# Kernel tuning notes

Hardware: AMD Instinct MI355X
Metric: run time of the kernel (lower is better)

## Reference

```python
import jax, jax.numpy as jnp
import numpy as np

N_EVENTS = 16
N_SAMPLES = 2 ** 15          # 32768
STEP = 256                   # window_size // 2
LONG_WINDOW = 4096
LONG_COEFFS = LONG_WINDOW // 2 + 1   # 2049
LONG_STEP = LONG_WINDOW // 2         # 2048
LONG_FRAMES = N_SAMPLES // LONG_STEP # 16
N_FRAMES = N_SAMPLES // STEP         # 128
B = 8                                 # audio batch
BE = B * N_EVENTS                     # event batch = 128


def setup_inputs() -> dict:
    key = jax.random.key(0)
    k1, k2, k3, k4 = jax.random.split(key, 4)
    env = jax.random.uniform(k1, (BE, LONG_WINDOW, LONG_FRAMES), jnp.float32)
    tf = jax.random.normal(k2, (BE, LONG_COEFFS * 2, LONG_FRAMES), jnp.float32)
    noise = jax.random.uniform(k3, (BE, LONG_WINDOW, LONG_FRAMES), jnp.float32)
    indices = jax.random.randint(k4, (B, N_EVENTS), 0, N_FRAMES, dtype=jnp.int32)
    return {"env": env, "tf": tf, "noise": noise, "indices": indices}


def _event_render(env, tf, noise):
    # env, noise: (BE, LONG_WINDOW, LONG_FRAMES); tf: (BE, 2*LONG_COEFFS, LONG_FRAMES)
    batch = env.shape[0]
    energy = env * (noise * 2.0 - 1.0)  # uniform_(-1, 1) noise scaled by amp

    # magnitude = norm over interleaved (real, imag) pairs, per torch view semantics
    pairs = tf.reshape(batch, LONG_COEFFS, 2, LONG_FRAMES)
    mag = jnp.sqrt(jnp.sum(pairs * pairs, axis=2))  # (batch, C, F)
    mx = jnp.max(mag.reshape(batch, -1), axis=-1, keepdims=True)
    mag = (mag.reshape(batch, -1) / (mx + 1e-8)).reshape(batch, LONG_COEFFS, LONG_FRAMES)
    imag = tf[:, LONG_COEFFS:, :]
    phase = jnp.arctan2(imag, mag) * np.pi  # torch.angle(complex(mag, imag)) * pi
    tfc = mag * jnp.exp(1j * phase)         # complex transfer fn (batch, C, F)

    # sequential per-frame recurrence: state feeds through rfft/irfft filtering
    e_t = jnp.transpose(energy, (2, 0, 1))  # (F, batch, W)
    t_t = jnp.transpose(tfc, (2, 0, 1))     # (F, batch, C)

    def step(prev, inp):
        e, t = inp
        local = prev + e
        spec = jnp.fft.rfft(local, axis=-1, norm='ortho') * t
        frame = jnp.fft.irfft(spec, n=LONG_WINDOW, axis=-1, norm='ortho')
        return frame, frame

    init = jnp.zeros((batch, LONG_WINDOW), energy.dtype)
    _, frames = jax.lax.scan(step, init, (e_t, t_t))   # (F, batch, W)
    frames = jnp.transpose(frames, (1, 0, 2))          # (batch, F, W)

    # overlap-add with hop = LONG_STEP = W/2: split frames into halves and add
    halves = frames.reshape(batch, LONG_FRAMES, 2, LONG_STEP)
    out = jnp.zeros((batch, LONG_FRAMES + 1, LONG_STEP), frames.dtype)
    out = out.at[:, :LONG_FRAMES].add(halves[:, :, 0])
    out = out.at[:, 1:].add(halves[:, :, 1])
    return out.reshape(batch, -1)[:, :N_SAMPLES]       # (BE, N_SAMPLES)


def _segment_render(atoms, indices):
    # atoms: (BE, N_SAMPLES) -> (B, N_EVENTS, N_SAMPLES); scatter-add at time offsets
    x = atoms.reshape(B, N_EVENTS, N_SAMPLES)
    times = indices * STEP                                      # (B, E)
    pos = times[:, :, None] + jnp.arange(N_SAMPLES)[None, None, :]  # (B, E, S)
    out = jnp.zeros((B, 2 * N_SAMPLES), x.dtype)
    bidx = jnp.arange(B)[:, None, None]
    out = out.at[bidx, pos].add(x)
    return out[:, None, :N_SAMPLES]                             # (B, 1, N_SAMPLES)


def reference(env, tf, noise, indices):
    atoms = _event_render(env, tf, noise)
    return _segment_render(atoms, indices)
```

## Files before the change

kernel.cpp:

```cpp
#include <hip/hip_runtime.h>
#include <hip/hip_fp16.h>
#include <math.h>

#define TWO_PI 6.283185307179586f

#define OFF_F    0ull
#define OFF_E    4194304ull
#define OFF_MAXP 8390656ull
#define OFF_Z    8391680ull

__device__ __forceinline__ int swz(int n) { return n ^ ((n >> 5) & 31); }

__device__ __forceinline__ int permf(int k) {
    return ((k & 1) << 10) | (((k >> 1) & 3) << 8) | (((k >> 3) & 3) << 6)
         | (((k >> 5) & 3) << 4) | (((k >> 7) & 3) << 2) | ((k >> 9) & 3);
}
__device__ __forceinline__ int perm8(int k) {
    return ((k & 7) << 8) | (((k >> 3) & 3) << 6) | (((k >> 5) & 3) << 4)
         | (((k >> 7) & 3) << 2) | ((k >> 9) & 3);
}

__device__ __forceinline__ float2 uph(unsigned u) {
    __half2 h = *(__half2*)&u;
    return __half22float2(h);
}
__device__ __forceinline__ unsigned pkh(float x, float y) {
    __half2 h = __floats2half2_rn(x, y);
    return *(unsigned*)&h;
}

__device__ __forceinline__ void r4f_core(float* cr, float* ci, int p0, int p1, int p2, int p3,
                                         float c1, float s1, float c2, float s2, float c3, float s3) {
    float ar = cr[p0], ai = ci[p0];
    float br = cr[p1], bi = ci[p1];
    float crr = cr[p2], cri = ci[p2];
    float drr = cr[p3], dri = ci[p3];
    float u0r = ar + crr, u0i = ai + cri;
    float u1r = ar - crr, u1i = ai - cri;
    float u2r = br + drr, u2i = bi + dri;
    float u3r = br - drr, u3i = bi - dri;
    cr[p0] = u0r + u2r; ci[p0] = u0i + u2i;
    float z1r = u1r + u3i, z1i = u1i - u3r;
    cr[p1] = z1r * c1 + z1i * s1; ci[p1] = z1i * c1 - z1r * s1;
    float z2r = u0r - u2r, z2i = u0i - u2i;
    cr[p2] = z2r * c2 + z2i * s2; ci[p2] = z2i * c2 - z2r * s2;
    float z3r = u1r - u3i, z3i = u1i + u3r;
    cr[p3] = z3r * c3 + z3i * s3; ci[p3] = z3i * c3 - z3r * s3;
}

__device__ __forceinline__ void r4i_pk(unsigned* b, int p0, int p1, int p2, int p3,
                                       float c1, float s1, float c2, float s2, float c3, float s3) {
    float2 z0 = uph(b[p0]), z1 = uph(b[p1]), z2 = uph(b[p2]), z3 = uph(b[p3]);
    float t1r = z1.x * c1 - z1.y * s1, t1i = z1.y * c1 + z1.x * s1;
    float t2r = z2.x * c2 - z2.y * s2, t2i = z2.y * c2 + z2.x * s2;
    float t3r = z3.x * c3 - z3.y * s3, t3i = z3.y * c3 + z3.x * s3;
    float u0r = z0.x + t2r, u0i = z0.y + t2i;
    float u1r = z0.x - t2r, u1i = z0.y - t2i;
    float u2r = t1r + t3r, u2i = t1i + t3i;
    float u3r = t1r - t3r, u3i = t1i - t3i;
    b[p0] = pkh(u0r + u2r, u0i + u2i);
    b[p1] = pkh(u1r - u3i, u1i + u3r);
    b[p2] = pkh(u0r - u2r, u0i - u2i);
    b[p3] = pkh(u1r + u3i, u1i - u3r);
}

#define STAGE4X(CORE, JEXPR, H, ANGEXPR)                                       \
    {                                                                          \
        _Pragma("unroll")                                                      \
        for (int half_ = 0; half_ < 2; ++half_) {                              \
            int b_ = tid + half_ * 1024;                                       \
            int i_ = b_ & 511;                                                 \
            float* cr_ = B + (b_ >> 9) * 4096;                                 \
            float* ci_ = cr_ + 2048;                                           \
            int j_ = (JEXPR);                                                  \
            int p0 = swz(j_), p1 = swz(j_ + (H)), p2 = swz(j_ + 2 * (H)),      \
                p3 = swz(j_ + 3 * (H));                                        \
            float s1, c1; __sincosf((ANGEXPR), &s1, &c1);                      \
            float c2 = c1 * c1 - s1 * s1, s2 = 2.f * c1 * s1;                  \
            float c3 = c1 * c2 - s1 * s2, s3 = s1 * c2 + c1 * s2;              \
            CORE(cr_, ci_, p0, p1, p2, p3, c1, s1, c2, s2, c3, s3);            \
        }                                                                      \
    }                                                                          \
    __syncthreads();

#define STAGE4P(JEXPR, H, ANGEXPR)                                             \
    {                                                                          \
        _Pragma("unroll")                                                      \
        for (int half_ = 0; half_ < 2; ++half_) {                              \
            int b_ = tid + half_ * 1024;                                       \
            int i_ = b_ & 511;                                                 \
            unsigned* bb_ = B2 + (b_ >> 9) * 2048;                             \
            int j_ = (JEXPR);                                                  \
            int p0 = swz(j_), p1 = swz(j_ + (H)), p2 = swz(j_ + 2 * (H)),      \
                p3 = swz(j_ + 3 * (H));                                        \
            float s1, c1; __sincosf((ANGEXPR), &s1, &c1);                      \
            float c2 = c1 * c1 - s1 * s1, s2 = 2.f * c1 * s1;                  \
            float c3 = c1 * c2 - s1 * s2, s3 = s1 * c2 + c1 * s2;              \
            r4i_pk(bb_, p0, p1, p2, p3, c1, s1, c2, s2, c3, s3);               \
        }                                                                      \
    }                                                                          \
    __syncthreads();

__global__ __launch_bounds__(1024, 8) void k_fwd(const float* __restrict__ env,
                                                 const float* __restrict__ noise,
                                                 const float* __restrict__ tf,
                                                 float* __restrict__ ws) {
    __shared__ float B[16384];
    int tid = threadIdx.x;
    int id = blockIdx.x;
    int xcd = id & 7, slot = id >> 3;
    int be = xcd * 16 + (slot >> 2);
    int fg = slot & 3;
    const float4* env4 = (const float4*)env;
    const float4* noi4 = (const float4*)noise;
    size_t base = (size_t)be * 16384 + fg;
#pragma unroll
    for (int it = 0; it < 4; ++it) {
        int n = it * 1024 + tid;
        float4 e = env4[base + (size_t)n * 4];
        float4 z = noi4[base + (size_t)n * 4];
        float v0 = e.x * (z.x * 2.0f - 1.0f);
        float v1 = e.y * (z.y * 2.0f - 1.0f);
        float v2 = e.z * (z.z * 2.0f - 1.0f);
        float v3 = e.w * (z.w * 2.0f - 1.0f);
        int m = swz(n >> 1) + (n & 1) * 2048;
        B[m] = v0; B[4096 + m] = v1; B[8192 + m] = v2; B[12288 + m] = v3;
    }
    __syncthreads();
    {
        int buf = tid >> 8, j = tid & 255;
        float* cr = B + buf * 4096;
        float* ci = cr + 2048;
        int p[8];
#pragma unroll
        for (int m = 0; m < 8; ++m) p[m] = swz(j + 256 * m);
        float xr[8], xi[8];
#pragma unroll
        for (int m = 0; m < 8; ++m) { xr[m] = cr[p[m]]; xi[m] = ci[p[m]]; }
        float t0r = xr[0] + xr[4], t0i = xi[0] + xi[4];
        float t1r = xr[0] - xr[4], t1i = xi[0] - xi[4];
        float t2r = xr[2] + xr[6], t2i = xi[2] + xi[6];
        float t3r = xr[2] - xr[6], t3i = xi[2] - xi[6];
        float A0r = t0r + t2r, A0i = t0i + t2i;
        float A2r = t0r - t2r, A2i = t0i - t2i;
        float A1r = t1r + t3i, A1i = t1i - t3r;
        float A3r = t1r - t3i, A3i = t1i + t3r;
        float u0r = xr[1] + xr[5], u0i = xi[1] + xi[5];
        float u1r = xr[1] - xr[5], u1i = xi[1] - xi[5];
        float u2r = xr[3] + xr[7], u2i = xi[3] + xi[7];
        float u3r = xr[3] - xr[7], u3i = xi[3] - xi[7];
        float B0r = u0r + u2r, B0i = u0i + u2i;
        float B2r = u0r - u2r, B2i = u0i - u2i;
        float B1r = u1r + u3i, B1i = u1i - u3r;
        float B3r = u1r - u3i, B3i = u1i + u3r;
        const float RH = 0.70710678118654752f;
        float b1r = (B1r + B1i) * RH, b1i = (B1i - B1r) * RH;
        float b2r = B2i, b2i = -B2r;
        float b3r = (B3i - B3r) * RH, b3i = -(B3r + B3i) * RH;
        float yr[8], yi[8];
        yr[0] = A0r + B0r; yi[0] = A0i + B0i; yr[4] = A0r - B0r; yi[4] = A0i - B0i;
        yr[1] = A1r + b1r; yi[1] = A1i + b1i; yr[5] = A1r - b1r; yi[5] = A1i - b1i;
        yr[2] = A2r + b2r; yi[2] = A2i + b2i; yr[6] = A2r - b2r; yi[6] = A2i - b2i;
        yr[3] = A3r + b3r; yi[3] = A3i + b3i; yr[7] = A3r - b3r; yi[7] = A3i - b3i;
        float s1, c1; __sincosf((float)j * (TWO_PI / 2048.0f), &s1, &c1);
        float wr = c1, wi = -s1;
        float cwr = wr, cwi = wi;
        cr[p[0]] = yr[0]; ci[p[0]] = yi[0];
#pragma unroll
        for (int m = 1; m < 8; ++m) {
            cr[p[m]] = yr[m] * cwr - yi[m] * cwi;
            ci[p[m]] = yr[m] * cwi + yi[m] * cwr;
            if (m < 7) {
                float nr = cwr * wr - cwi * wi;
                cwi = cwr * wi + cwi * wr;
                cwr = nr;
            }
        }
    }
    __syncthreads();
    STAGE4X(r4f_core, (i_ >> 6) * 256 + (i_ & 63), 64, (float)(i_ & 63) * (TWO_PI / 256.0f));
    STAGE4X(r4f_core, (i_ & 31) * 64 + (i_ >> 5), 16, (float)(i_ >> 5) * (TWO_PI / 64.0f));
    STAGE4X(r4f_core, (i_ & 127) * 16 + (i_ >> 7), 4, (float)(i_ >> 7) * (TWO_PI / 16.0f));
    STAGE4X(r4f_core, i_ * 4, 1, 0.0f);
    __half2* Ebase = (__half2*)(ws + OFF_E) + (size_t)(be * 16 + fg * 4) * 2049;
    for (int k = tid; k <= 1024; k += 1024) {
        int pk = swz(perm8(k));
        int pm = swz(perm8((2048 - k) & 2047));
        float s4, c4; __sincosf((float)k * (TWO_PI / 4096.0f), &s4, &c4);
#pragma unroll
        for (int j4 = 0; j4 < 4; ++j4) {
            float* cr = B + j4 * 4096;
            float* ci = cr + 2048;
            float zkr = cr[pk], zki = ci[pk], zmr = cr[pm], zmi = ci[pm];
            float xer = 0.5f * (zkr + zmr), xei = 0.5f * (zki - zmi);
            float xor_ = 0.5f * (zki + zmi), xoi = 0.5f * (zmr - zkr);
            float wr = xor_ * c4 + xoi * s4;
            float wi = xoi * c4 - xor_ * s4;
            __half2* Eg = Ebase + (size_t)j4 * 2049;
            Eg[k] = __floats2half2_rn(xer + wr, xei + wi);
            Eg[2048 - k] = __floats2half2_rn(xer - wr, wi - xei);
        }
    }
    __syncthreads();
    const float4* ab4 = (const float4*)(tf + (size_t)be * 65568);
    int b0 = fg * 513;
    int nb = (fg == 3) ? 510 : 513;
    float mx = 0.f;
    for (int u = tid; u < nb * 4; u += 1024) {
        int g = u >> 2, e = u & 3;
        int bin = b0 + g;
        float4 A = ab4[bin * 8 + e];
        float4 Bv = ab4[bin * 8 + e + 4];
        mx = fmaxf(mx, fmaxf(fmaxf(A.x * A.x + Bv.x * Bv.x, A.y * A.y + Bv.y * Bv.y),
                             fmaxf(A.z * A.z + Bv.z * Bv.z, A.w * A.w + Bv.w * Bv.w)));
    }
#pragma unroll
    for (int off = 32; off > 0; off >>= 1)
        mx = fmaxf(mx, __shfl_xor(mx, off));
    if ((tid & 63) == 0) B[tid >> 6] = mx;
    __syncthreads();
    if (tid == 0) {
        float m = B[0];
#pragma unroll
        for (int i = 1; i < 16; ++i) m = fmaxf(m, B[i]);
        ws[OFF_MAXP + be * 4 + fg] = m;
    }
}

__global__ __launch_bounds__(256) void k_recur(const float* __restrict__ tf,
                                               float* __restrict__ ws) {
    __shared__ float sm2lo[256 * 17], simlo[256 * 17];
    __shared__ float sm2hi[256 * 17], simhi[256 * 17];
    int tid = threadIdx.x;
    int be = blockIdx.y;
    int k0 = blockIdx.x << 8;
    int hi0 = 1793 - k0;
    const float* tfb = tf + (size_t)be * 65568;
    const float4* ab4 = (const float4*)tfb;
    const float4* im4 = (const float4*)(tfb + 32784);

    for (int u = tid; u < 2048; u += 256) {
        int half = u >> 10, v = u & 1023;
        int g = v >> 2, e = v & 3;
        int bin = half ? (hi0 + g) : (k0 + g);
        float4 A = ab4[bin * 8 + e];
        float4 Bv = ab4[bin * 8 + e + 4];
        float4 I = im4[bin * 4 + e];
        int o = g * 17 + e * 4;
        float* sm = half ? sm2hi : sm2lo;
        float* si = half ? simhi : simlo;
        sm[o + 0] = A.x * A.x + Bv.x * Bv.x;
        sm[o + 1] = A.y * A.y + Bv.y * Bv.y;
        sm[o + 2] = A.z * A.z + Bv.z * Bv.z;
        sm[o + 3] = A.w * A.w + Bv.w * Bv.w;
        si[o + 0] = I.x; si[o + 1] = I.y; si[o + 2] = I.z; si[o + 3] = I.w;
    }
    __syncthreads();

    int k = k0 + tid;
    int m = 2048 - k;
    int rhi = 255 - tid;
    const float* mp = ws + OFF_MAXP + be * 4;
    float m2x = fmaxf(fmaxf(mp[0], mp[1]), fmaxf(mp[2], mp[3]));
    float rden = 1.0f / (sqrtf(m2x) + 1e-8f);
    const __half2* Eb = (const __half2*)(ws + OFF_E) + (size_t)be * 16 * 2049;
    __half2* Zb = (__half2*)(ws + OFF_Z) + (size_t)be * 16 * 2048;
    float2 evlo[16], evhi[16];
#pragma unroll
    for (int f = 0; f < 16; ++f) {
        evlo[f] = __half22float2(Eb[(size_t)f * 2049 + k]);
        evhi[f] = __half22float2(Eb[(size_t)f * 2049 + m]);
    }
    float ym = (k == 0) ? 0.0f : 1.0f;
    float s4, c4; __sincosf((float)k * (TWO_PI / 4096.0f), &s4, &c4);
    const float SCL = 1.0f / 2048.0f;
    float srl = 0.f, sil = 0.f, srh = 0.f, sih = 0.f;
#pragma unroll
    for (int f = 0; f < 16; ++f) {
        float mh = sqrtf(sm2lo[tid * 17 + f]) * rden;
        float ph = atan2f(simlo[tid * 17 + f], mh) * 3.14159265358979f;
        float sp, cp; __sincosf(ph, &sp, &cp);
        float Tr = mh * cp, Ti = mh * sp;
        sil *= ym;
        srl += evlo[f].x; sil += evlo[f].y;
        float nr = srl * Tr - sil * Ti;
        sil = srl * Ti + sil * Tr; srl = nr;
        float mh2 = sqrtf(sm2hi[rhi * 17 + f]) * rden;
        float ph2 = atan2f(simhi[rhi * 17 + f], mh2) * 3.14159265358979f;
        float sp2, cp2; __sincosf(ph2, &sp2, &cp2);
        float Tr2 = mh2 * cp2, Ti2 = mh2 * sp2;
        sih *= ym;
        srh += evhi[f].x; sih += evhi[f].y;
        float nr2 = srh * Tr2 - sih * Ti2;
        sih = srh * Ti2 + sih * Tr2; srh = nr2;
        __half2* Zf = Zb + (size_t)f * 2048;
        if (k == 0) {
            float y0 = srl * SCL, yn = srh * SCL;
            Zf[0] = __floats2half2_rn(0.5f * (y0 + yn), 0.5f * (y0 - yn));
        } else {
            float ykr = srl * SCL, yki = sil * SCL;
            float ymr = srh * SCL, ymi = sih * SCL;
            float er = 0.5f * (ykr + ymr), ei = 0.5f * (yki - ymi);
            float dr = ykr - ymr, di = yki + ymi;
            float orr = 0.5f * (dr * c4 - di * s4);
            float oi = 0.5f * (dr * s4 + di * c4);
            Zf[k] = __floats2half2_rn(er - oi, ei + orr);
            Zf[m] = __floats2half2_rn(er + oi, orr - ei);
        }
    }
    if (k0 == 0 && tid == 0) {
        float sr = 0.f, si = 0.f;
#pragma unroll
        for (int f = 0; f < 16; ++f) {
            float a = tfb[1024 * 32 + f];
            float b = tfb[1024 * 32 + 16 + f];
            float im = tfb[32784 + 1024 * 16 + f];
            float mh = sqrtf(a * a + b * b) * rden;
            float ph = atan2f(im, mh) * 3.14159265358979f;
            float sp, cp; __sincosf(ph, &sp, &cp);
            float Tr = mh * cp, Ti = mh * sp;
            float2 e = __half22float2(Eb[(size_t)f * 2049 + 1024]);
            sr += e.x; si += e.y;
            float nr = sr * Tr - si * Ti;
            si = sr * Ti + si * Tr; sr = nr;
            Zb[(size_t)f * 2048 + 1024] = __floats2half2_rn(sr * SCL, -si * SCL);
        }
    }
}

__global__ __launch_bounds__(1024, 8) void k_fft_inv(float* __restrict__ ws) {
    __shared__ unsigned B2[8192];
    int tid = threadIdx.x;
    int be = blockIdx.x >> 2, fg = blockIdx.x & 3;
    const __half2* Zbase = (const __half2*)(ws + OFF_Z) + (size_t)(be * 16 + fg * 4) * 2048;
    {
        int n0 = tid * 2;
        int p0 = swz(permf(n0)), p1 = swz(permf(n0 + 1));
#pragma unroll
        for (int j4 = 0; j4 < 4; ++j4) {
            uint2 raw = ((const uint2*)(Zbase + (size_t)j4 * 2048))[tid];
            unsigned* bb = B2 + j4 * 2048;
            bb[p0] = raw.x;
            bb[p1] = raw.y;
        }
    }
    __syncthreads();
    STAGE4P(i_ * 4, 1, 0.0f);
    STAGE4P((i_ & 127) * 16 + (i_ >> 7), 4, (float)(i_ >> 7) * (TWO_PI / 16.0f));
    STAGE4P((i_ & 31) * 64 + (i_ >> 5), 16, (float)(i_ >> 5) * (TWO_PI / 64.0f));
    STAGE4P((i_ >> 6) * 256 + (i_ & 63), 64, (float)(i_ & 63) * (TWO_PI / 256.0f));
    STAGE4P((i_ >> 8) * 1024 + (i_ & 255), 256, (float)(i_ & 255) * (TWO_PI / 1024.0f));
    {
        int sj = swz(tid), sjb = swz(tid + 1024);
        float s, c; __sincosf((float)tid * (TWO_PI / 2048.0f), &s, &c);
        __half2* Fbase = (__half2*)(ws + OFF_F) + (size_t)(be * 16 + fg * 4) * 2048;
#pragma unroll
        for (int j4 = 0; j4 < 4; ++j4) {
            unsigned* bb = B2 + j4 * 2048;
            float2 a = uph(bb[sj]);
            float2 b = uph(bb[sjb]);
            float tr = b.x * c - b.y * s, ti2 = b.x * s + b.y * c;
            __half2* Fg = Fbase + (size_t)j4 * 2048;
            Fg[tid] = __floats2half2_rn(a.x + tr, a.y + ti2);
            Fg[tid + 1024] = __floats2half2_rn(a.x - tr, a.y - ti2);
        }
    }
}

__global__ __launch_bounds__(256) void k_segment(const float* __restrict__ ws,
                                                 const int* __restrict__ indices,
                                                 float* __restrict__ out) {
    __shared__ int ste[16];
    int tid = threadIdx.x;
    int b = blockIdx.y;
    if (tid < 16) ste[tid] = indices[b * 16 + tid] * 256;
    __syncthreads();
    int g = blockIdx.x * 256 + tid;
    int t = g << 2;
    const __half* F = (const __half*)(ws + OFF_F);
    float4 acc = make_float4(0.f, 0.f, 0.f, 0.f);
#pragma unroll
    for (int e = 0; e < 16; ++e) {
        int te = ste[e];
        if (t >= te) {
            int d = t - te;
            int j = d >> 11, r = d & 2047;
            size_t base = (size_t)(b * 16 + e) * 65536;
            uint2 raw = *(const uint2*)(F + base + j * 4096 + r);
            float2 a0 = __half22float2(*(const __half2*)&raw.x);
            float2 a1 = __half22float2(*(const __half2*)&raw.y);
            acc.x += a0.x; acc.y += a0.y; acc.z += a1.x; acc.w += a1.y;
            if (j >= 1) {
                uint2 rw2 = *(const uint2*)(F + base + (j - 1) * 4096 + 2048 + r);
                float2 b0 = __half22float2(*(const __half2*)&rw2.x);
                float2 b1 = __half22float2(*(const __half2*)&rw2.y);
                acc.x += b0.x; acc.y += b0.y; acc.z += b1.x; acc.w += b1.y;
            }
        }
    }
    ((float4*)out)[(size_t)b * 8192 + g] = acc;
}

extern "C" void kernel_launch(void* const* d_in, const int* in_sizes, int n_in,
                              void* d_out, int out_size, void* d_ws, size_t ws_size,
                              hipStream_t stream) {
    const float* env = (const float*)d_in[0];
    const float* tf = (const float*)d_in[1];
    const float* noise = (const float*)d_in[2];
    const int* indices = (const int*)d_in[3];
    float* ws = (float*)d_ws;
    float* out = (float*)d_out;

    k_fwd<<<dim3(512), dim3(1024), 0, stream>>>(env, noise, tf, ws);
    k_recur<<<dim3(4, 128), dim3(256), 0, stream>>>(tf, ws);
    k_fft_inv<<<dim3(512), dim3(1024), 0, stream>>>(ws);
    k_segment<<<dim3(32, 8), dim3(256), 0, stream>>>(ws, indices, out);
}
```

Measured before the change: 74.08 us.

## Split forward FFT kernel into 1024 blocks of 512 threads handling two frames each

```diff
diff --git a/kernel.cpp b/kernel.cpp
--- a/kernel.cpp
+++ b/kernel.cpp
@@ -64,11 +64,11 @@
     b[p3] = pkh(u1r + u3i, u1i - u3r);
 }
 
-#define STAGE4X(CORE, JEXPR, H, ANGEXPR)                                       \
+#define STAGE2F(JEXPR, H, ANGEXPR)                                             \
     {                                                                          \
         _Pragma("unroll")                                                      \
         for (int half_ = 0; half_ < 2; ++half_) {                              \
-            int b_ = tid + half_ * 1024;                                       \
+            int b_ = tid + half_ * 512;                                        \
             int i_ = b_ & 511;                                                 \
             float* cr_ = B + (b_ >> 9) * 4096;                                 \
             float* ci_ = cr_ + 2048;                                           \
@@ -78,7 +78,7 @@
             float s1, c1; __sincosf((ANGEXPR), &s1, &c1);                      \
             float c2 = c1 * c1 - s1 * s1, s2 = 2.f * c1 * s1;                  \
             float c3 = c1 * c2 - s1 * s2, s3 = s1 * c2 + c1 * s2;              \
-            CORE(cr_, ci_, p0, p1, p2, p3, c1, s1, c2, s2, c3, s3);            \
+            r4f_core(cr_, ci_, p0, p1, p2, p3, c1, s1, c2, s2, c3, s3);        \
         }                                                                      \
     }                                                                          \
     __syncthreads();
@@ -101,30 +101,30 @@
     }                                                                          \
     __syncthreads();
 
-__global__ __launch_bounds__(1024, 8) void k_fwd(const float* __restrict__ env,
-                                                 const float* __restrict__ noise,
-                                                 const float* __restrict__ tf,
-                                                 float* __restrict__ ws) {
-    __shared__ float B[16384];
+__global__ __launch_bounds__(512, 8) void k_fwd(const float* __restrict__ env,
+                                                const float* __restrict__ noise,
+                                                const float* __restrict__ tf,
+                                                float* __restrict__ ws) {
+    __shared__ float B[8192];
     int tid = threadIdx.x;
     int id = blockIdx.x;
     int xcd = id & 7, slot = id >> 3;
-    int be = xcd * 16 + (slot >> 2);
-    int fg = slot & 3;
+    int be = xcd * 16 + (slot >> 3);
+    int fh = slot & 7;
+    int q = fh >> 1, sel = fh & 1;
     const float4* env4 = (const float4*)env;
     const float4* noi4 = (const float4*)noise;
-    size_t base = (size_t)be * 16384 + fg;
-#pragma unroll
-    for (int it = 0; it < 4; ++it) {
-        int n = it * 1024 + tid;
+    size_t base = (size_t)be * 16384 + q;
+#pragma unroll
+    for (int it = 0; it < 8; ++it) {
+        int n = it * 512 + tid;
         float4 e = env4[base + (size_t)n * 4];
         float4 z = noi4[base + (size_t)n * 4];
-        float v0 = e.x * (z.x * 2.0f - 1.0f);
-        float v1 = e.y * (z.y * 2.0f - 1.0f);
-        float v2 = e.z * (z.z * 2.0f - 1.0f);
-        float v3 = e.w * (z.w * 2.0f - 1.0f);
+        float v0, v1;
+        if (sel == 0) { v0 = e.x * (z.x * 2.f - 1.f); v1 = e.y * (z.y * 2.f - 1.f); }
+        else          { v0 = e.z * (z.z * 2.f - 1.f); v1 = e.w * (z.w * 2.f - 1.f); }
         int m = swz(n >> 1) + (n & 1) * 2048;
-        B[m] = v0; B[4096 + m] = v1; B[8192 + m] = v2; B[12288 + m] = v3;
+        B[m] = v0; B[4096 + m] = v1;
     }
     __syncthreads();
     {
@@ -178,35 +178,39 @@
         }
     }
     __syncthreads();
-    STAGE4X(r4f_core, (i_ >> 6) * 256 + (i_ & 63), 64, (float)(i_ & 63) * (TWO_PI / 256.0f));
-    STAGE4X(r4f_core, (i_ & 31) * 64 + (i_ >> 5), 16, (float)(i_ >> 5) * (TWO_PI / 64.0f));
-    STAGE4X(r4f_core, (i_ & 127) * 16 + (i_ >> 7), 4, (float)(i_ >> 7) * (TWO_PI / 16.0f));
-    STAGE4X(r4f_core, i_ * 4, 1, 0.0f);
-    __half2* Ebase = (__half2*)(ws + OFF_E) + (size_t)(be * 16 + fg * 4) * 2049;
-    for (int k = tid; k <= 1024; k += 1024) {
-        int pk = swz(perm8(k));
-        int pm = swz(perm8((2048 - k) & 2047));
-        float s4, c4; __sincosf((float)k * (TWO_PI / 4096.0f), &s4, &c4);
-#pragma unroll
-        for (int j4 = 0; j4 < 4; ++j4) {
-            float* cr = B + j4 * 4096;
-            float* ci = cr + 2048;
-            float zkr = cr[pk], zki = ci[pk], zmr = cr[pm], zmi = ci[pm];
-            float xer = 0.5f * (zkr + zmr), xei = 0.5f * (zki - zmi);
-            float xor_ = 0.5f * (zki + zmi), xoi = 0.5f * (zmr - zkr);
-            float wr = xor_ * c4 + xoi * s4;
-            float wi = xoi * c4 - xor_ * s4;
-            __half2* Eg = Ebase + (size_t)j4 * 2049;
-            Eg[k] = __floats2half2_rn(xer + wr, xei + wi);
-            Eg[2048 - k] = __floats2half2_rn(xer - wr, wi - xei);
+    STAGE2F((i_ >> 6) * 256 + (i_ & 63), 64, (float)(i_ & 63) * (TWO_PI / 256.0f));
+    STAGE2F((i_ & 31) * 64 + (i_ >> 5), 16, (float)(i_ >> 5) * (TWO_PI / 64.0f));
+    STAGE2F((i_ & 127) * 16 + (i_ >> 7), 4, (float)(i_ >> 7) * (TWO_PI / 16.0f));
+    STAGE2F(i_ * 4, 1, 0.0f);
+    __half2* Ebase = (__half2*)(ws + OFF_E) + (size_t)(be * 16 + fh * 2) * 2049;
+#pragma unroll
+    for (int it = 0; it < 3; ++it) {
+        int k = tid + it * 512;
+        if (k <= 1024) {
+            int pk = swz(perm8(k));
+            int pm = swz(perm8((2048 - k) & 2047));
+            float s4, c4; __sincosf((float)k * (TWO_PI / 4096.0f), &s4, &c4);
+#pragma unroll
+            for (int j2 = 0; j2 < 2; ++j2) {
+                float* cr = B + j2 * 4096;
+                float* ci = cr + 2048;
+                float zkr = cr[pk], zki = ci[pk], zmr = cr[pm], zmi = ci[pm];
+                float xer = 0.5f * (zkr + zmr), xei = 0.5f * (zki - zmi);
+                float xor_ = 0.5f * (zki + zmi), xoi = 0.5f * (zmr - zkr);
+                float wr = xor_ * c4 + xoi * s4;
+                float wi = xoi * c4 - xor_ * s4;
+                __half2* Eg = Ebase + (size_t)j2 * 2049;
+                Eg[k] = __floats2half2_rn(xer + wr, xei + wi);
+                Eg[2048 - k] = __floats2half2_rn(xer - wr, wi - xei);
+            }
         }
     }
     __syncthreads();
     const float4* ab4 = (const float4*)(tf + (size_t)be * 65568);
-    int b0 = fg * 513;
-    int nb = (fg == 3) ? 510 : 513;
+    int b0 = fh * 257;
+    int nb = (fh == 7) ? 250 : 257;
     float mx = 0.f;
-    for (int u = tid; u < nb * 4; u += 1024) {
+    for (int u = tid; u < nb * 4; u += 512) {
         int g = u >> 2, e = u & 3;
         int bin = b0 + g;
         float4 A = ab4[bin * 8 + e];
@@ -222,8 +226,8 @@
     if (tid == 0) {
         float m = B[0];
 #pragma unroll
-        for (int i = 1; i < 16; ++i) m = fmaxf(m, B[i]);
-        ws[OFF_MAXP + be * 4 + fg] = m;
+        for (int i = 1; i < 8; ++i) m = fmaxf(m, B[i]);
+        ws[OFF_MAXP + be * 8 + fh] = m;
     }
 }
 
@@ -260,8 +264,9 @@
     int k = k0 + tid;
     int m = 2048 - k;
     int rhi = 255 - tid;
-    const float* mp = ws + OFF_MAXP + be * 4;
-    float m2x = fmaxf(fmaxf(mp[0], mp[1]), fmaxf(mp[2], mp[3]));
+    const float* mp = ws + OFF_MAXP + be * 8;
+    float m2x = fmaxf(fmaxf(fmaxf(mp[0], mp[1]), fmaxf(mp[2], mp[3])),
+                      fmaxf(fmaxf(mp[4], mp[5]), fmaxf(mp[6], mp[7])));
     float rden = 1.0f / (sqrtf(m2x) + 1e-8f);
     const __half2* Eb = (const __half2*)(ws + OFF_E) + (size_t)be * 16 * 2049;
     __half2* Zb = (__half2*)(ws + OFF_Z) + (size_t)be * 16 * 2048;
@@ -411,7 +416,7 @@
     float* ws = (float*)d_ws;
     float* out = (float*)d_out;
 
-    k_fwd<<<dim3(512), dim3(1024), 0, stream>>>(env, noise, tf, ws);
+    k_fwd<<<dim3(1024), dim3(512), 0, stream>>>(env, noise, tf, ws);
     k_recur<<<dim3(4, 128), dim3(256), 0, stream>>>(tf, ws);
     k_fft_inv<<<dim3(512), dim3(1024), 0, stream>>>(ws);
     k_segment<<<dim3(32, 8), dim3(256), 0, stream>>>(ws, indices, out);
```

Result: slower. 90.19 us (+21.7%).
